# Kernel tuning notes

Hardware: AMD Instinct MI355X
Metric: run time of the kernel (lower is better)

Reference implementation:

```python
import jax, jax.numpy as jnp
import numpy as np

N, T, D, H = 100000, 16, 8, 40
HP1 = H + 1
ALPHA_DP = 1.0
KAPPA0 = 1000.0   # priorGaussianVarKappa
NU0 = 100.0       # priorWishartNu
PSI0_SCALE = 500.0  # priorWishartPsi = 500*I


def setup_inputs() -> dict:
    key = jax.random.key(0)
    ks = jax.random.split(key, 6)
    return {
        "BetaGamma1": jnp.ones((1, T), jnp.float32),
        "Phi": jax.random.uniform(ks[0], (N, T), jnp.float32),
        "inputData": jax.random.normal(ks[1], (N, D), jnp.float32),
        "outputData": jax.random.normal(ks[2], (N, 1), jnp.float32),
        "weightELM": jax.random.uniform(ks[3], (D, H), jnp.float32) * 2.0 - 1.0,
        "biasELM": jax.random.normal(ks[4], (H, 1), jnp.float32),
        "epsilonA": jnp.ones((1, T), jnp.float32),
        "epsilonB": jnp.ones((1, T), jnp.float32),
        "zetaA": 1e-4 * jnp.ones((1, T), jnp.float32),
        "zetaB": jnp.ones((1, T), jnp.float32),
    }


def reference(BetaGamma1, Phi, inputData, outputData, weightELM, biasELM,
              epsilonA, epsilonB, zetaA, zetaB):
    f32 = jnp.float32
    mu0 = jnp.zeros((D, 1), f32)                      # priorGaussianMeanMu
    Psi0 = PSI0_SCALE * jnp.eye(D, dtype=f32)         # priorWishartPsi

    sumPhi = jnp.sum(Phi, axis=0, keepdims=True)      # [1,T]

    # stick-breaking Beta params. Torch builds a flipped [T,N,T] tril mask;
    # mathematically BetaGamma2[t] = alpha + sum_{j>t} sum_n Phi[n,j]
    BetaGamma1_new = jnp.ones_like(BetaGamma1) + sumPhi
    col = sumPhi[0]                                   # [T]
    rev_incl = jnp.cumsum(col[::-1])[::-1]            # sum_{j>=t}
    BetaGamma2 = (ALPHA_DP + (rev_incl - col))[None, :]

    # Gaussian-Wishart natural-parameter updates.
    # Torch loops over clusters doing [N,D,D] bmm outer products; this is
    # S[:,:,t] = sum_n Phi[n,t] x_n x_n^T
    S = jnp.einsum('nt,ni,nj->ijt', Phi, inputData, inputData)  # [D,D,T]
    t11 = -0.5 * (Psi0 + KAPPA0 * mu0 @ mu0.T)[:, :, None] - 0.5 * S
    t12 = KAPPA0 * mu0 + inputData.T @ Phi            # [D,T]
    t21 = -0.5 * sumPhi - 0.5 * (NU0 + D + 2)         # [1,T]
    kappa = KAPPA0 + sumPhi                           # [1,T]
    mu = t12 / kappa                                  # [D,T]
    nu = -2.0 * t21 - 2.0 - float(D)                  # [1,T]
    psi = -2.0 * t11 - kappa[0][None, None, :] * jnp.einsum('it,jt->ijt', mu, mu)

    # ELM feature map + augmented design matrix X = [sigmoid(x W + b), 1]
    hmap = jax.nn.sigmoid(inputData @ weightELM + biasELM.T)   # [N,H]
    X = jnp.concatenate([hmap, jnp.ones((inputData.shape[0], 1), f32)], axis=1)  # [N,HP1]

    epsExp = (epsilonA / epsilonB)[0]                 # [T]
    zetaExp = (zetaA / zetaB)[0]                      # [T]

    # A[t] = X^T diag(Phi[:,t]) X   (torch: per-cluster bmm with diag_embed)
    A = jnp.einsum('nt,ni,nj->tij', Phi, X, X)        # [T,HP1,HP1]
    WS = jnp.linalg.inv(epsExp[:, None, None] * A
                        + zetaExp[:, None, None] * jnp.eye(HP1, dtype=f32))
    # b[t] = X^T diag(Phi[:,t]) y
    b = jnp.einsum('ni,nt->ti', X * outputData, Phi)  # [T,HP1]
    WMv = zetaExp[:, None] * jnp.einsum('tij,tj->ti', WS, b)   # [T,HP1]
    WM = WMv[:, :, None]                              # [T,HP1,1]

    # prior Zeta/Epsilon alias the variational initial values in __init__
    zetaA_new = zetaA + (H + 1) * 0.5
    zetaB_new = zetaB + 0.5 * (jnp.sum(WMv * WMv, axis=1)
                               + jnp.trace(WS, axis1=-2, axis2=-1))[None, :]
    epsA_new = epsilonA + 0.5 * sumPhi

    pred = jnp.einsum('ni,ti->tn', X, WMv)            # [T,N]
    err = outputData.T - pred                          # [T,N]
    t1 = jnp.einsum('tn,nt->t', err * err, Phi)[None, :]
    t2 = jnp.einsum('tij,tji->t', A, WS)[None, :]
    epsB_new = epsilonB + 0.5 * (t1 + t2)

    return (BetaGamma1_new, BetaGamma2, mu, kappa, nu, psi,
            WM, WS, zetaA_new, zetaB_new, epsA_new, epsB_new)
```

## Files before the change

kernel.cpp:

```cpp
#include <hip/hip_runtime.h>

#define Nn 100000
#define Tt 16
#define Dd 8
#define Hh 40
#define HP1 41

#define CSZ 53248
#define XET_OFF  0
#define XET_SZ   (64 * Nn)
#define PHIT_OFF (XET_OFF + XET_SZ)
#define PHIT_SZ  (16 * Nn)
#define ACC_OFF  (PHIT_OFF + PHIT_SZ)
#define PART_OFF (ACC_OFF + CSZ)
#define P_OFF    (PART_OFF + 8 * CSZ)

#define OFF_BG1   0
#define OFF_BG2   16
#define OFF_MU    32
#define OFF_KAPPA 160
#define OFF_NU    176
#define OFF_PSI   192
#define OFF_WM    1216
#define OFF_WS    1872
#define OFF_ZA    28768
#define OFF_ZB    28784
#define OFF_EA    28800
#define OFF_EB    28816

typedef _Float16 f16x8 __attribute__((ext_vector_type(8)));
typedef float f32x4 __attribute__((ext_vector_type(4)));
typedef unsigned short u16x8 __attribute__((ext_vector_type(8)));
typedef unsigned int u32x4 __attribute__((ext_vector_type(4)));

#define AIDX(i, t, j) ((((i) * 16 + (t)) * 64) + (j))

__global__ __launch_bounds__(256)
void elm_expand(const float* __restrict__ Phi, const float* __restrict__ Xd,
                const float* __restrict__ Yd, const float* __restrict__ W,
                const float* __restrict__ bb, unsigned int* __restrict__ XeT,
                float* __restrict__ PhiT)
{
  __shared__ float sW[Dd * Hh];
  __shared__ float sb[Hh];
  __shared__ float xs[64][9];
  __shared__ float ys[64];
  __shared__ float hrow[64][41];
  __shared__ float pt[16][68];
  int tid = threadIdx.x;
  int n0 = blockIdx.x * 64;

  for (int i = tid; i < Dd * Hh; i += 256) sW[i] = W[i];
  if (tid < Hh) sb[tid] = bb[tid];
  if (tid < 128) {
    int nl = tid >> 1, h4 = (tid & 1) * 4;
    int gn = n0 + nl;
    float4 v = (gn < Nn) ? *(const float4*)(Xd + (size_t)gn * 8 + h4)
                         : make_float4(0.f, 0.f, 0.f, 0.f);
    xs[nl][h4 + 0] = v.x; xs[nl][h4 + 1] = v.y;
    xs[nl][h4 + 2] = v.z; xs[nl][h4 + 3] = v.w;
  }
  if (tid < 64) { int gn = n0 + tid; ys[tid] = (gn < Nn) ? Yd[gn] : 0.f; }
  {
    int nl = tid >> 2, q = tid & 3;
    int gn = n0 + nl;
    float4 v = (gn < Nn) ? *(const float4*)(Phi + (size_t)gn * 16 + q * 4)
                         : make_float4(0.f, 0.f, 0.f, 0.f);
    pt[q * 4 + 0][nl] = v.x; pt[q * 4 + 1][nl] = v.y;
    pt[q * 4 + 2][nl] = v.z; pt[q * 4 + 3][nl] = v.w;
  }
  __syncthreads();
  {
    int nl = tid >> 2, hq = (tid & 3) * 10;
    for (int hh = 0; hh < 10; ++hh) {
      int h = hq + hh;
      float z = sb[h];
#pragma unroll
      for (int d = 0; d < 8; ++d) z = fmaf(xs[nl][d], sW[d * Hh + h], z);
      hrow[nl][h] = 1.f / (1.f + __expf(-z));
    }
  }
  __syncthreads();
  {
    int t = tid & 15, nq = tid >> 4;
    int gn = n0 + nq * 4;
    if (gn < Nn) {
      float4 v = make_float4(pt[t][nq * 4 + 0], pt[t][nq * 4 + 1],
                             pt[t][nq * 4 + 2], pt[t][nq * 4 + 3]);
      *(float4*)(PhiT + (size_t)t * Nn + gn) = v;
    }
  }
  {
    int c = tid >> 2, nb = (tid & 3) * 16;
    for (int q = 0; q < 4; ++q) {
      int nl = nb + q * 4;
      int gn = n0 + nl;
      if (gn >= Nn) break;
      unsigned int pu[4];
#pragma unroll
      for (int j = 0; j < 4; ++j) {
        int n = nl + j;
        float v;
        if (c < Hh) v = hrow[n][c];
        else if (c == 40) v = 1.f;
        else if (c < 49) v = xs[n][c - 41];
        else if (c == 49) v = ys[n];
        else v = 0.f;
        _Float16 hi = (_Float16)v;
        _Float16 lo = (_Float16)(v - (float)hi);
        pu[j] = ((unsigned int)__builtin_bit_cast(unsigned short, lo) << 16)
              |  (unsigned int)__builtin_bit_cast(unsigned short, hi);
      }
      *(uint4*)(XeT + (size_t)c * Nn + gn) =
          make_uint4(pu[0], pu[1], pu[2], pu[3]);
    }
  }
}

__device__ __forceinline__ void gload16(const void* g, void* l) {
  __builtin_amdgcn_global_load_lds(
      (const __attribute__((address_space(1))) unsigned int*)g,
      (__attribute__((address_space(3))) unsigned int*)l, 16, 0, 0);
}

__device__ __forceinline__ void unpack8(u32x4 a, u32x4 b, f16x8& hi, f16x8& lo) {
  u16x8 vh, vl;
#pragma unroll
  for (int e = 0; e < 4; ++e) {
    vh[e] = (unsigned short)(a[e] & 0xffffu);
    vl[e] = (unsigned short)(a[e] >> 16);
    vh[4 + e] = (unsigned short)(b[e] & 0xffffu);
    vl[4 + e] = (unsigned short)(b[e] >> 16);
  }
  hi = __builtin_bit_cast(f16x8, vh);
  lo = __builtin_bit_cast(f16x8, vl);
}

__device__ __forceinline__ void buildA(u32x4 a, u32x4 b, const float* ph,
                                       f16x8& ah, f16x8& al) {
  unsigned int u8[8];
#pragma unroll
  for (int e = 0; e < 4; ++e) { u8[e] = a[e]; u8[4 + e] = b[e]; }
#pragma unroll
  for (int e = 0; e < 8; ++e) {
    unsigned int u = u8[e];
    float hi = (float)__builtin_bit_cast(_Float16, (unsigned short)(u & 0xffffu));
    float lo = (float)__builtin_bit_cast(_Float16, (unsigned short)(u >> 16));
    float v = ph[e] * (hi + lo);
    _Float16 h = (_Float16)v;
    ah[e] = h;
    al[e] = (_Float16)(v - (float)h);
  }
}

__global__ __launch_bounds__(256, 2)
void gram_mfma(const float* __restrict__ PhiT, const unsigned int* __restrict__ XeT,
               float* __restrict__ P, int CH)
{
  __shared__ __align__(16) unsigned int xe_lds[2][2048];
  __shared__ __align__(16) float phi_lds[2][512];

  int tid = threadIdx.x;
  int l = tid & 63, w = tid >> 6;
  int lr = l >> 3, lp = l & 7;
  int gsw = lp ^ lr;
  int l15 = l & 15, lg = l >> 4;
  int bM = blockIdx.x, c = blockIdx.y;
  int n0 = c * CH;
  int rem = Nn - n0; if (rem > CH) rem = CH;
  int nsteps = rem >> 5;
  int i0 = bM * 13;

  const unsigned int* gx0 = XeT + (size_t)(16 * w + lr) * Nn + n0 + 4 * gsw;
  const unsigned int* gx1 = XeT + (size_t)(16 * w + 8 + lr) * Nn + n0 + 4 * gsw;
  const float* gp = PhiT + (size_t)(8 * w + lr) * Nn + n0 + 4 * gsw;

#define STAGE(nxt) do {                                   \
    gload16(gx0, &xe_lds[nxt][(2 * w) * 256]);            \
    gload16(gx1, &xe_lds[nxt][(2 * w + 1) * 256]);        \
    if (w < 2) gload16(gp, &phi_lds[nxt][w * 256]);       \
    gx0 += 32; gx1 += 32; gp += 32;                       \
  } while (0)

  int s1 = (2 * lg) ^ (l15 & 7), s2 = (2 * lg + 1) ^ (l15 & 7);
  int off_p0 = (l15 * 32 + 4 * s1) * 4, off_p1 = (l15 * 32 + 4 * s2) * 4;
  int off_b0[4], off_b1[4];
#pragma unroll
  for (int nt = 0; nt < 4; ++nt) {
    off_b0[nt] = ((l15 + 16 * nt) * 32 + 4 * s1) * 4;
    off_b1[nt] = ((l15 + 16 * nt) * 32 + 4 * s2) * 4;
  }
  int off_a0[4], off_a1[4];
#pragma unroll
  for (int mi = 0; mi < 4; ++mi) {
    int i = i0 + 4 * w + mi;
    int a1 = (2 * lg) ^ (i & 7), a2 = (2 * lg + 1) ^ (i & 7);
    off_a0[mi] = (i * 32 + 4 * a1) * 4;
    off_a1[mi] = (i * 32 + 4 * a2) * 4;
  }

  f32x4 acc[4][4];
#pragma unroll
  for (int mi = 0; mi < 4; ++mi)
#pragma unroll
    for (int nt = 0; nt < 4; ++nt) acc[mi][nt] = (f32x4){0.f, 0.f, 0.f, 0.f};

  STAGE(0);
  __syncthreads();

  for (int s = 0; s < nsteps; ++s) {
    int cur = s & 1;
    if (s + 1 < nsteps) STAGE(cur ^ 1);

    const char* xb = (const char*)&xe_lds[cur][0];
    const char* pb = (const char*)&phi_lds[cur][0];
    f32x4 p0 = *(const f32x4*)(pb + off_p0);
    f32x4 p1 = *(const f32x4*)(pb + off_p1);
    float ph[8] = {p0[0], p0[1], p0[2], p0[3], p1[0], p1[1], p1[2], p1[3]};

    f16x8 bh[4], bl[4];
#pragma unroll
    for (int nt = 0; nt < 4; ++nt) {
      u32x4 lo4 = *(const u32x4*)(xb + off_b0[nt]);
      u32x4 hi4 = *(const u32x4*)(xb + off_b1[nt]);
      unpack8(lo4, hi4, bh[nt], bl[nt]);
    }
#pragma unroll
    for (int mi = 0; mi < 4; ++mi) {
      u32x4 a0 = *(const u32x4*)(xb + off_a0[mi]);
      u32x4 a1 = *(const u32x4*)(xb + off_a1[mi]);
      f16x8 ah, al;
      buildA(a0, a1, ph, ah, al);
#pragma unroll
      for (int nt = 0; nt < 4; ++nt) {
        acc[mi][nt] = __builtin_amdgcn_mfma_f32_16x16x32_f16(ah, bh[nt], acc[mi][nt], 0, 0, 0);
        acc[mi][nt] = __builtin_amdgcn_mfma_f32_16x16x32_f16(ah, bl[nt], acc[mi][nt], 0, 0, 0);
        acc[mi][nt] = __builtin_amdgcn_mfma_f32_16x16x32_f16(al, bh[nt], acc[mi][nt], 0, 0, 0);
      }
    }
    __syncthreads();
  }
#undef STAGE

  float* Pc = P + (size_t)c * CSZ;
#pragma unroll
  for (int mi = 0; mi < 4; ++mi) {
    int mloc = 4 * w + mi;
    if (mloc < 13) {
      int i = i0 + mloc;
#pragma unroll
      for (int nt = 0; nt < 4; ++nt) {
        int j = nt * 16 + l15;
#pragma unroll
        for (int r = 0; r < 4; ++r)
          Pc[(i * 16 + lg * 4 + r) * 64 + j] = acc[mi][nt][r];
      }
    }
  }
}

__global__ __launch_bounds__(256)
void reduce_a(const float4* __restrict__ P4, int nchunks, float4* __restrict__ part4)
{
  int g = blockIdx.y;
  int idx = blockIdx.x * 256 + threadIdx.x;
  int per = (nchunks + 7) / 8;
  int c0 = g * per, c1 = c0 + per; if (c1 > nchunks) c1 = nchunks;
  float4 s = make_float4(0.f, 0.f, 0.f, 0.f);
  for (int cc = c0; cc < c1; ++cc) {
    float4 v = P4[(size_t)cc * (CSZ / 4) + idx];
    s.x += v.x; s.y += v.y; s.z += v.z; s.w += v.w;
  }
  part4[(size_t)g * (CSZ / 4) + idx] = s;
}

__global__ __launch_bounds__(256)
void reduce_b(const float4* __restrict__ part4, float4* __restrict__ acc4)
{
  int idx = blockIdx.x * 256 + threadIdx.x;
  float4 s = make_float4(0.f, 0.f, 0.f, 0.f);
#pragma unroll
  for (int g = 0; g < 8; ++g) {
    float4 v = part4[(size_t)g * (CSZ / 4) + idx];
    s.x += v.x; s.y += v.y; s.z += v.z; s.w += v.w;
  }
  acc4[idx] = s;
}

__global__ __launch_bounds__(256)
void finalize_kernel(const float* __restrict__ acc, const float* __restrict__ epsA,
                     const float* __restrict__ epsB, const float* __restrict__ zetA,
                     const float* __restrict__ zetB, float* __restrict__ out)
{
  int t = blockIdx.x;
  int tid = threadIdx.x;
  __shared__ float G[HP1][84];
  __shared__ float As[HP1][HP1 + 1];
  __shared__ float bs[HP1];
  __shared__ float colk[HP1];
  __shared__ float red[256];
  __shared__ float wmv[HP1];
  __shared__ float rowv[4][HP1 + 1];
  __shared__ float mus[Dd];

  float epsExp = epsA[t] / epsB[t];
  float zetaExp = zetA[t] / zetB[t];

  for (int idx = tid; idx < HP1 * HP1; idx += 256) {
    int i = idx / HP1, j = idx % HP1;
    float a = acc[AIDX(i, t, j)];
    As[i][j] = a;
    G[i][j] = epsExp * a + (i == j ? zetaExp : 0.f);
    G[i][41 + j] = (i == j) ? 1.f : 0.f;
  }
  for (int idx = tid; idx < HP1; idx += 256) {
    G[idx][82] = 0.f; G[idx][83] = 0.f;
    bs[idx] = acc[AIDX(idx, t, 49)];
  }
  __syncthreads();

  int c = tid % HP1;
  int ig = tid / HP1;
  int irow0 = ig * 7;

  for (int k = 0; k < HP1; ++k) {
    float pivinv = 1.f / G[k][k];
    if (tid >= 1 && tid <= HP1) G[k][k + tid] *= pivinv;
    if (tid < HP1) colk[tid] = (tid == k) ? 0.f : G[tid][k];
    __syncthreads();
    if (ig < 6) {
      int j = k + 1 + c;
      float pk = G[k][j];
#pragma unroll
      for (int r = 0; r < 7; ++r) {
        int i = irow0 + r;
        if (i < HP1 && i != k) G[i][j] = fmaf(-colk[i], pk, G[i][j]);
      }
    }
    __syncthreads();
  }

  for (int idx = tid; idx < HP1 * HP1; idx += 256) {
    int i = idx / HP1, j = idx % HP1;
    out[OFF_WS + (t * HP1 + i) * HP1 + j] = G[i][41 + j];
  }
  if (tid < HP1) {
    float s = 0.f;
    for (int j = 0; j < HP1; ++j) s += G[tid][41 + j] * bs[j];
    float w = zetaExp * s;
    wmv[tid] = w;
    out[OFF_WM + t * HP1 + tid] = w;
  }
  __syncthreads();
  float lt2 = 0.f;
  for (int idx = tid; idx < HP1 * HP1; idx += 256) {
    int i = idx / HP1, j = idx % HP1;
    lt2 += As[i][j] * G[i][41 + j];
  }
  red[tid] = lt2; __syncthreads();
  for (int s = 128; s > 0; s >>= 1) {
    if (tid < s) red[tid] += red[tid + s];
    __syncthreads();
  }
  float t2v = red[0];
  if (tid < HP1) {
    float w = wmv[tid];
    float aw = 0.f;
    for (int j = 0; j < HP1; ++j) aw += As[tid][j] * wmv[j];
    rowv[0][tid] = w * bs[tid];
    rowv[1][tid] = w * w;
    rowv[2][tid] = G[tid][41 + tid];
    rowv[3][tid] = w * aw;
  }
  __syncthreads();

  float sp = acc[AIDX(40, t, 40)];
  float kap = 1000.f + sp;
  float syy = acc[AIDX(49, t, 49)];

  if (tid == 0) {
    float wb = 0.f, wn = 0.f, trc = 0.f, quad = 0.f;
    for (int i = 0; i < HP1; ++i) {
      wb += rowv[0][i]; wn += rowv[1][i]; trc += rowv[2][i]; quad += rowv[3][i];
    }
    float t1 = syy - 2.f * wb + quad;
    out[OFF_BG1 + t] = 1.f + sp;
    float rest = 0.f;
    for (int u = t + 1; u < Tt; ++u) rest += acc[AIDX(40, u, 40)];
    out[OFF_BG2 + t] = 1.f + rest;
    out[OFF_KAPPA + t] = kap;
    out[OFF_NU + t] = sp + 100.f;
    out[OFF_ZA + t] = zetA[t] + 0.5f * (float)HP1;
    out[OFF_ZB + t] = zetB[t] + 0.5f * (wn + trc);
    out[OFF_EA + t] = epsA[t] + 0.5f * sp;
    out[OFF_EB + t] = epsB[t] + 0.5f * (t1 + t2v);
  }
  if (tid < Dd) {
    float m = acc[AIDX(40, t, 41 + tid)] / kap;
    mus[tid] = m;
    out[OFF_MU + tid * Tt + t] = m;
  }
  __syncthreads();
  if (tid < Dd * Dd) {
    int i = tid / Dd, j = tid % Dd;
    float S = acc[AIDX(41 + i, t, 41 + j)];
    float v = (i == j ? 500.f : 0.f) + S - kap * mus[i] * mus[j];
    out[OFF_PSI + (i * Dd + j) * Tt + t] = v;
  }
}

extern "C" void kernel_launch(void* const* d_in, const int* in_sizes, int n_in,
                              void* d_out, int out_size, void* d_ws, size_t ws_size,
                              hipStream_t stream) {
  const float* Phi = (const float*)d_in[1];
  const float* Xd  = (const float*)d_in[2];
  const float* Yd  = (const float*)d_in[3];
  const float* W   = (const float*)d_in[4];
  const float* bb  = (const float*)d_in[5];
  const float* eA  = (const float*)d_in[6];
  const float* eB  = (const float*)d_in[7];
  const float* zA  = (const float*)d_in[8];
  const float* zB  = (const float*)d_in[9];
  float* out = (float*)d_out;
  float* ws  = (float*)d_ws;

  unsigned int* XeT = (unsigned int*)(ws + XET_OFF);
  float* PhiT    = ws + PHIT_OFF;
  float* acc_red = ws + ACC_OFF;
  float* part    = ws + PART_OFF;
  float* P       = ws + P_OFF;

  long maxChunks = ((long)(ws_size / 4) - (long)P_OFF) / CSZ;
  if (maxChunks < 1) maxChunks = 1;
  long sp = (3125 + maxChunks - 1) / maxChunks;
  if (sp < 13) sp = 13;
  int CH = (int)(32 * sp);
  int KCe = (Nn + CH - 1) / CH;

  hipLaunchKernelGGL(elm_expand, dim3((Nn + 63) / 64), dim3(256), 0, stream,
                     Phi, Xd, Yd, W, bb, XeT, PhiT);
  hipLaunchKernelGGL(gram_mfma, dim3(4, KCe), dim3(256), 0, stream,
                     PhiT, XeT, P, CH);
  hipLaunchKernelGGL(reduce_a, dim3(52, 8), dim3(256), 0, stream,
                     (const float4*)P, KCe, (float4*)part);
  hipLaunchKernelGGL(reduce_b, dim3(52), dim3(256), 0, stream,
                     (const float4*)part, (float4*)acc_red);
  hipLaunchKernelGGL(finalize_kernel, dim3(Tt), dim3(256), 0, stream,
                     acc_red, eA, eB, zA, zB, out);
}
```

Before: 186.0 us.

## Split expanded features into fp32, hi and lo planes; fuse final reduction into finalize

The expand kernel now writes separate fp32, fp16-hi and fp16-lo planes, so the Gram kernel loads B fragments directly instead of unpacking them. The A side is built from fp32 times Phi using packed conversions, and only the 13 rows each block needs are staged. The grid is remapped to 1D so that chunks sharing a row block are interleaved. The reduce_b launch is removed and finalize sums the 8 partials itself. This trades extra workspace and expand-kernel write traffic for less ALU work in the inner loop and one fewer launch.

```diff
diff --git a/kernel.cpp b/kernel.cpp
--- a/kernel.cpp
+++ b/kernel.cpp
@@ -7,12 +7,11 @@
 #define HP1 41
 
 #define CSZ 53248
-#define XET_OFF  0
-#define XET_SZ   (64 * Nn)
-#define PHIT_OFF (XET_OFF + XET_SZ)
-#define PHIT_SZ  (16 * Nn)
-#define ACC_OFF  (PHIT_OFF + PHIT_SZ)
-#define PART_OFF (ACC_OFF + CSZ)
+#define XEF_OFF  0
+#define XEH_OFF  (XEF_OFF + 64 * Nn)
+#define XEL_OFF  (XEH_OFF + 32 * Nn)
+#define PHIT_OFF (XEL_OFF + 32 * Nn)
+#define PART_OFF (PHIT_OFF + 16 * Nn)
 #define P_OFF    (PART_OFF + 8 * CSZ)
 
 #define OFF_BG1   0
@@ -30,7 +29,6 @@
 
 typedef _Float16 f16x8 __attribute__((ext_vector_type(8)));
 typedef float f32x4 __attribute__((ext_vector_type(4)));
-typedef unsigned short u16x8 __attribute__((ext_vector_type(8)));
 typedef unsigned int u32x4 __attribute__((ext_vector_type(4)));
 
 #define AIDX(i, t, j) ((((i) * 16 + (t)) * 64) + (j))
@@ -38,7 +36,8 @@
 __global__ __launch_bounds__(256)
 void elm_expand(const float* __restrict__ Phi, const float* __restrict__ Xd,
                 const float* __restrict__ Yd, const float* __restrict__ W,
-                const float* __restrict__ bb, unsigned int* __restrict__ XeT,
+                const float* __restrict__ bb, float* __restrict__ XeF32,
+                unsigned short* __restrict__ XeHi, unsigned short* __restrict__ XeLo,
                 float* __restrict__ PhiT)
 {
   __shared__ float sW[Dd * Hh];
@@ -91,28 +90,52 @@
     }
   }
   {
-    int c = tid >> 2, nb = (tid & 3) * 16;
-    for (int q = 0; q < 4; ++q) {
-      int nl = nb + q * 4;
-      int gn = n0 + nl;
-      if (gn >= Nn) break;
-      unsigned int pu[4];
-#pragma unroll
-      for (int j = 0; j < 4; ++j) {
-        int n = nl + j;
-        float v;
-        if (c < Hh) v = hrow[n][c];
-        else if (c == 40) v = 1.f;
-        else if (c < 49) v = xs[n][c - 41];
-        else if (c == 49) v = ys[n];
-        else v = 0.f;
-        _Float16 hi = (_Float16)v;
-        _Float16 lo = (_Float16)(v - (float)hi);
-        pu[j] = ((unsigned int)__builtin_bit_cast(unsigned short, lo) << 16)
-              |  (unsigned int)__builtin_bit_cast(unsigned short, hi);
+    int cidx = tid >> 2, seg = tid & 3;
+    int nl0 = seg * 16;
+    float vv[16];
+#pragma unroll
+    for (int j = 0; j < 16; ++j) {
+      int n = nl0 + j;
+      float v;
+      if (cidx < Hh) v = hrow[n][cidx];
+      else if (cidx == 40) v = 1.f;
+      else if (cidx < 49) v = xs[n][cidx - 41];
+      else if (cidx == 49) v = ys[n];
+      else v = 0.f;
+      vv[j] = v;
+    }
+#pragma unroll
+    for (int q2 = 0; q2 < 4; ++q2) {
+      int gn = n0 + nl0 + q2 * 4;
+      if (gn < Nn)
+        *(float4*)(XeF32 + (size_t)cidx * Nn + gn) =
+            make_float4(vv[q2 * 4], vv[q2 * 4 + 1], vv[q2 * 4 + 2], vv[q2 * 4 + 3]);
+    }
+    unsigned short hs[16], ls[16];
+#pragma unroll
+    for (int j = 0; j < 16; ++j) {
+      _Float16 h = (_Float16)vv[j];
+      float r = vv[j] - (float)h;
+      _Float16 lo = (_Float16)r;
+      hs[j] = __builtin_bit_cast(unsigned short, h);
+      ls[j] = __builtin_bit_cast(unsigned short, lo);
+    }
+#pragma unroll
+    for (int q2 = 0; q2 < 2; ++q2) {
+      int gn = n0 + nl0 + q2 * 8;
+      if (gn < Nn) {
+        uint4 uh, ul;
+        uh.x = hs[q2*8+0] | ((unsigned)hs[q2*8+1] << 16);
+        uh.y = hs[q2*8+2] | ((unsigned)hs[q2*8+3] << 16);
+        uh.z = hs[q2*8+4] | ((unsigned)hs[q2*8+5] << 16);
+        uh.w = hs[q2*8+6] | ((unsigned)hs[q2*8+7] << 16);
+        ul.x = ls[q2*8+0] | ((unsigned)ls[q2*8+1] << 16);
+        ul.y = ls[q2*8+2] | ((unsigned)ls[q2*8+3] << 16);
+        ul.z = ls[q2*8+4] | ((unsigned)ls[q2*8+5] << 16);
+        ul.w = ls[q2*8+6] | ((unsigned)ls[q2*8+7] << 16);
+        *(uint4*)(XeHi + (size_t)cidx * Nn + gn) = uh;
+        *(uint4*)(XeLo + (size_t)cidx * Nn + gn) = ul;
       }
-      *(uint4*)(XeT + (size_t)c * Nn + gn) =
-          make_uint4(pu[0], pu[1], pu[2], pu[3]);
     }
   }
 }
@@ -123,81 +146,77 @@
       (__attribute__((address_space(3))) unsigned int*)l, 16, 0, 0);
 }
 
-__device__ __forceinline__ void unpack8(u32x4 a, u32x4 b, f16x8& hi, f16x8& lo) {
-  u16x8 vh, vl;
-#pragma unroll
-  for (int e = 0; e < 4; ++e) {
-    vh[e] = (unsigned short)(a[e] & 0xffffu);
-    vl[e] = (unsigned short)(a[e] >> 16);
-    vh[4 + e] = (unsigned short)(b[e] & 0xffffu);
-    vl[4 + e] = (unsigned short)(b[e] >> 16);
-  }
-  hi = __builtin_bit_cast(f16x8, vh);
-  lo = __builtin_bit_cast(f16x8, vl);
-}
-
-__device__ __forceinline__ void buildA(u32x4 a, u32x4 b, const float* ph,
-                                       f16x8& ah, f16x8& al) {
-  unsigned int u8[8];
-#pragma unroll
-  for (int e = 0; e < 4; ++e) { u8[e] = a[e]; u8[4 + e] = b[e]; }
-#pragma unroll
-  for (int e = 0; e < 8; ++e) {
-    unsigned int u = u8[e];
-    float hi = (float)__builtin_bit_cast(_Float16, (unsigned short)(u & 0xffffu));
-    float lo = (float)__builtin_bit_cast(_Float16, (unsigned short)(u >> 16));
-    float v = ph[e] * (hi + lo);
-    _Float16 h = (_Float16)v;
-    ah[e] = h;
-    al[e] = (_Float16)(v - (float)h);
-  }
-}
-
 __global__ __launch_bounds__(256, 2)
-void gram_mfma(const float* __restrict__ PhiT, const unsigned int* __restrict__ XeT,
-               float* __restrict__ P, int CH)
+void gram_mfma(const float* __restrict__ PhiT, const float* __restrict__ XeF32,
+               const unsigned short* __restrict__ XeHi,
+               const unsigned short* __restrict__ XeLo,
+               float* __restrict__ P, int CH, int KCe)
 {
-  __shared__ __align__(16) unsigned int xe_lds[2][2048];
-  __shared__ __align__(16) float phi_lds[2][512];
+  __shared__ __align__(16) char smem[2][12288];
+
+  int id = blockIdx.x;
+  int low3 = id & 7, rest = id >> 3;
+  int bM = rest & 3, chigh = rest >> 2;
+  int c = chigh * 8 + low3;
+  if (c >= KCe) return;
 
   int tid = threadIdx.x;
   int l = tid & 63, w = tid >> 6;
-  int lr = l >> 3, lp = l & 7;
-  int gsw = lp ^ lr;
   int l15 = l & 15, lg = l >> 4;
-  int bM = blockIdx.x, c = blockIdx.y;
   int n0 = c * CH;
   int rem = Nn - n0; if (rem > CH) rem = CH;
   int nsteps = rem >> 5;
   int i0 = bM * 13;
 
-  const unsigned int* gx0 = XeT + (size_t)(16 * w + lr) * Nn + n0 + 4 * gsw;
-  const unsigned int* gx1 = XeT + (size_t)(16 * w + 8 + lr) * Nn + n0 + 4 * gsw;
-  const float* gp = PhiT + (size_t)(8 * w + lr) * Nn + n0 + 4 * gsw;
-
-#define STAGE(nxt) do {                                   \
-    gload16(gx0, &xe_lds[nxt][(2 * w) * 256]);            \
-    gload16(gx1, &xe_lds[nxt][(2 * w + 1) * 256]);        \
-    if (w < 2) gload16(gp, &phi_lds[nxt][w * 256]);       \
-    gx0 += 32; gx1 += 32; gp += 32;                       \
+  const char* gp[3];
+  int gstep[3];
+  int ldoff[3];
+  {
+    int idq = w * 3;
+#pragma unroll
+    for (int q = 0; q < 3; ++q) {
+      int sid = idq + q;
+      ldoff[q] = sid * 1024;
+      if (sid < 8) {
+        int qq = sid & 3;
+        int row = 16 * qq + (l >> 2);
+        int g = (l & 3) ^ ((l >> 3) & 3);
+        const unsigned short* basep = (sid < 4) ? XeHi : XeLo;
+        gp[q] = (const char*)(basep + (size_t)row * Nn + n0 + 8 * g);
+        gstep[q] = 64;
+      } else if (sid < 10) {
+        int qq = sid - 8;
+        int row = 8 * qq + (l >> 3);
+        gp[q] = (const char*)(XeF32 + (size_t)(i0 + row) * Nn + n0 + 4 * (l & 7));
+        gstep[q] = 128;
+      } else {
+        int qq = sid - 10;
+        int row = 8 * qq + (l >> 3);
+        int g = (l & 7) ^ (l >> 3);
+        gp[q] = (const char*)(PhiT + (size_t)row * Nn + n0 + 4 * g);
+        gstep[q] = 128;
+      }
+    }
+  }
+
+#define STAGE(buf) do {                          \
+    char* db = &smem[buf][0];                    \
+    gload16(gp[0], db + ldoff[0]); gp[0] += gstep[0]; \
+    gload16(gp[1], db + ldoff[1]); gp[1] += gstep[1]; \
+    gload16(gp[2], db + ldoff[2]); gp[2] += gstep[2]; \
   } while (0)
 
-  int s1 = (2 * lg) ^ (l15 & 7), s2 = (2 * lg + 1) ^ (l15 & 7);
-  int off_p0 = (l15 * 32 + 4 * s1) * 4, off_p1 = (l15 * 32 + 4 * s2) * 4;
-  int off_b0[4], off_b1[4];
-#pragma unroll
-  for (int nt = 0; nt < 4; ++nt) {
-    off_b0[nt] = ((l15 + 16 * nt) * 32 + 4 * s1) * 4;
-    off_b1[nt] = ((l15 + 16 * nt) * 32 + 4 * s2) * 4;
-  }
-  int off_a0[4], off_a1[4];
-#pragma unroll
-  for (int mi = 0; mi < 4; ++mi) {
-    int i = i0 + 4 * w + mi;
-    int a1 = (2 * lg) ^ (i & 7), a2 = (2 * lg + 1) ^ (i & 7);
-    off_a0[mi] = (i * 32 + 4 * a1) * 4;
-    off_a1[mi] = (i * 32 + 4 * a2) * 4;
-  }
+  int sB = (l15 >> 1) & 3;
+  int off_b[4];
+#pragma unroll
+  for (int nt = 0; nt < 4; ++nt)
+    off_b[nt] = (l15 + 16 * nt) * 64 + 16 * (lg ^ sB);
+  int off_a[4];
+#pragma unroll
+  for (int mi = 0; mi < 4; ++mi)
+    off_a[mi] = 8192 + (4 * w + mi) * 128 + 32 * lg;
+  int off_p0 = 10240 + l15 * 128 + 16 * ((2 * lg) ^ (l15 & 7));
+  int off_p1 = 10240 + l15 * 128 + 16 * ((2 * lg + 1) ^ (l15 & 7));
 
   f32x4 acc[4][4];
 #pragma unroll
@@ -212,25 +231,41 @@
     int cur = s & 1;
     if (s + 1 < nsteps) STAGE(cur ^ 1);
 
-    const char* xb = (const char*)&xe_lds[cur][0];
-    const char* pb = (const char*)&phi_lds[cur][0];
-    f32x4 p0 = *(const f32x4*)(pb + off_p0);
-    f32x4 p1 = *(const f32x4*)(pb + off_p1);
-    float ph[8] = {p0[0], p0[1], p0[2], p0[3], p1[0], p1[1], p1[2], p1[3]};
-
+    const char* base = &smem[cur][0];
+    f32x4 p0 = *(const f32x4*)(base + off_p0);
+    f32x4 p1 = *(const f32x4*)(base + off_p1);
     f16x8 bh[4], bl[4];
 #pragma unroll
     for (int nt = 0; nt < 4; ++nt) {
-      u32x4 lo4 = *(const u32x4*)(xb + off_b0[nt]);
-      u32x4 hi4 = *(const u32x4*)(xb + off_b1[nt]);
-      unpack8(lo4, hi4, bh[nt], bl[nt]);
+      bh[nt] = *(const f16x8*)(base + off_b[nt]);
+      bl[nt] = *(const f16x8*)(base + 4096 + off_b[nt]);
     }
 #pragma unroll
     for (int mi = 0; mi < 4; ++mi) {
-      u32x4 a0 = *(const u32x4*)(xb + off_a0[mi]);
-      u32x4 a1 = *(const u32x4*)(xb + off_a1[mi]);
-      f16x8 ah, al;
-      buildA(a0, a1, ph, ah, al);
+      f32x4 x0 = *(const f32x4*)(base + off_a[mi]);
+      f32x4 x1 = *(const f32x4*)(base + off_a[mi] + 16);
+      float v0 = p0[0] * x0[0], v1 = p0[1] * x0[1];
+      float v2 = p0[2] * x0[2], v3 = p0[3] * x0[3];
+      float v4 = p1[0] * x1[0], v5 = p1[1] * x1[1];
+      float v6 = p1[2] * x1[2], v7 = p1[3] * x1[3];
+      auto h0 = __builtin_amdgcn_cvt_pkrtz(v0, v1);
+      auto h1 = __builtin_amdgcn_cvt_pkrtz(v2, v3);
+      auto h2 = __builtin_amdgcn_cvt_pkrtz(v4, v5);
+      auto h3 = __builtin_amdgcn_cvt_pkrtz(v6, v7);
+      float r0 = v0 - (float)h0[0], r1 = v1 - (float)h0[1];
+      float r2 = v2 - (float)h1[0], r3 = v3 - (float)h1[1];
+      float r4 = v4 - (float)h2[0], r5 = v5 - (float)h2[1];
+      float r6 = v6 - (float)h3[0], r7 = v7 - (float)h3[1];
+      auto e0 = __builtin_amdgcn_cvt_pkrtz(r0, r1);
+      auto e1 = __builtin_amdgcn_cvt_pkrtz(r2, r3);
+      auto e2 = __builtin_amdgcn_cvt_pkrtz(r4, r5);
+      auto e3 = __builtin_amdgcn_cvt_pkrtz(r6, r7);
+      u32x4 uh = {__builtin_bit_cast(unsigned int, h0), __builtin_bit_cast(unsigned int, h1),
+                  __builtin_bit_cast(unsigned int, h2), __builtin_bit_cast(unsigned int, h3)};
+      u32x4 ul = {__builtin_bit_cast(unsigned int, e0), __builtin_bit_cast(unsigned int, e1),
+                  __builtin_bit_cast(unsigned int, e2), __builtin_bit_cast(unsigned int, e3)};
+      f16x8 ah = __builtin_bit_cast(f16x8, uh);
+      f16x8 al = __builtin_bit_cast(f16x8, ul);
 #pragma unroll
       for (int nt = 0; nt < 4; ++nt) {
         acc[mi][nt] = __builtin_amdgcn_mfma_f32_16x16x32_f16(ah, bh[nt], acc[mi][nt], 0, 0, 0);
@@ -274,21 +309,15 @@
   part4[(size_t)g * (CSZ / 4) + idx] = s;
 }
 
+__device__ __forceinline__ float accv(const float* __restrict__ part, int idx) {
+  float s = 0.f;
+#pragma unroll
+  for (int g = 0; g < 8; ++g) s += part[g * CSZ + idx];
+  return s;
+}
+
 __global__ __launch_bounds__(256)
-void reduce_b(const float4* __restrict__ part4, float4* __restrict__ acc4)
-{
-  int idx = blockIdx.x * 256 + threadIdx.x;
-  float4 s = make_float4(0.f, 0.f, 0.f, 0.f);
-#pragma unroll
-  for (int g = 0; g < 8; ++g) {
-    float4 v = part4[(size_t)g * (CSZ / 4) + idx];
-    s.x += v.x; s.y += v.y; s.z += v.z; s.w += v.w;
-  }
-  acc4[idx] = s;
-}
-
-__global__ __launch_bounds__(256)
-void finalize_kernel(const float* __restrict__ acc, const float* __restrict__ epsA,
+void finalize_kernel(const float* __restrict__ part, const float* __restrict__ epsA,
                      const float* __restrict__ epsB, const float* __restrict__ zetA,
                      const float* __restrict__ zetB, float* __restrict__ out)
 {
@@ -308,14 +337,14 @@
 
   for (int idx = tid; idx < HP1 * HP1; idx += 256) {
     int i = idx / HP1, j = idx % HP1;
-    float a = acc[AIDX(i, t, j)];
+    float a = accv(part, AIDX(i, t, j));
     As[i][j] = a;
     G[i][j] = epsExp * a + (i == j ? zetaExp : 0.f);
     G[i][41 + j] = (i == j) ? 1.f : 0.f;
   }
   for (int idx = tid; idx < HP1; idx += 256) {
     G[idx][82] = 0.f; G[idx][83] = 0.f;
-    bs[idx] = acc[AIDX(idx, t, 49)];
+    bs[idx] = accv(part, AIDX(idx, t, 49));
   }
   __syncthreads();
 
@@ -374,9 +403,9 @@
   }
   __syncthreads();
 
-  float sp = acc[AIDX(40, t, 40)];
+  float sp = accv(part, AIDX(40, t, 40));
   float kap = 1000.f + sp;
-  float syy = acc[AIDX(49, t, 49)];
+  float syy = accv(part, AIDX(49, t, 49));
 
   if (tid == 0) {
     float wb = 0.f, wn = 0.f, trc = 0.f, quad = 0.f;
@@ -386,7 +415,7 @@
     float t1 = syy - 2.f * wb + quad;
     out[OFF_BG1 + t] = 1.f + sp;
     float rest = 0.f;
-    for (int u = t + 1; u < Tt; ++u) rest += acc[AIDX(40, u, 40)];
+    for (int u = t + 1; u < Tt; ++u) rest += accv(part, AIDX(40, u, 40));
     out[OFF_BG2 + t] = 1.f + rest;
     out[OFF_KAPPA + t] = kap;
     out[OFF_NU + t] = sp + 100.f;
@@ -396,14 +425,14 @@
     out[OFF_EB + t] = epsB[t] + 0.5f * (t1 + t2v);
   }
   if (tid < Dd) {
-    float m = acc[AIDX(40, t, 41 + tid)] / kap;
+    float m = accv(part, AIDX(40, t, 41 + tid)) / kap;
     mus[tid] = m;
     out[OFF_MU + tid * Tt + t] = m;
   }
   __syncthreads();
   if (tid < Dd * Dd) {
     int i = tid / Dd, j = tid % Dd;
-    float S = acc[AIDX(41 + i, t, 41 + j)];
+    float S = accv(part, AIDX(41 + i, t, 41 + j));
     float v = (i == j ? 500.f : 0.f) + S - kap * mus[i] * mus[j];
     out[OFF_PSI + (i * Dd + j) * Tt + t] = v;
   }
@@ -424,11 +453,12 @@
   float* out = (float*)d_out;
   float* ws  = (float*)d_ws;
 
-  unsigned int* XeT = (unsigned int*)(ws + XET_OFF);
-  float* PhiT    = ws + PHIT_OFF;
-  float* acc_red = ws + ACC_OFF;
-  float* part    = ws + PART_OFF;
-  float* P       = ws + P_OFF;
+  float* XeF32 = ws + XEF_OFF;
+  unsigned short* XeHi = (unsigned short*)(ws + XEH_OFF);
+  unsigned short* XeLo = (unsigned short*)(ws + XEL_OFF);
+  float* PhiT = ws + PHIT_OFF;
+  float* part = ws + PART_OFF;
+  float* P    = ws + P_OFF;
 
   long maxChunks = ((long)(ws_size / 4) - (long)P_OFF) / CSZ;
   if (maxChunks < 1) maxChunks = 1;
@@ -436,15 +466,14 @@
   if (sp < 13) sp = 13;
   int CH = (int)(32 * sp);
   int KCe = (Nn + CH - 1) / CH;
+  int grid1 = 32 * ((KCe + 7) / 8);
 
   hipLaunchKernelGGL(elm_expand, dim3((Nn + 63) / 64), dim3(256), 0, stream,
-                     Phi, Xd, Yd, W, bb, XeT, PhiT);
-  hipLaunchKernelGGL(gram_mfma, dim3(4, KCe), dim3(256), 0, stream,
-                     PhiT, XeT, P, CH);
+                     Phi, Xd, Yd, W, bb, XeF32, XeHi, XeLo, PhiT);
+  hipLaunchKernelGGL(gram_mfma, dim3(grid1), dim3(256), 0, stream,
+                     PhiT, XeF32, XeHi, XeLo, P, CH, KCe);
   hipLaunchKernelGGL(reduce_a, dim3(52, 8), dim3(256), 0, stream,
                      (const float4*)P, KCe, (float4*)part);
-  hipLaunchKernelGGL(reduce_b, dim3(52), dim3(256), 0, stream,
-                     (const float4*)part, (float4*)acc_red);
   hipLaunchKernelGGL(finalize_kernel, dim3(Tt), dim3(256), 0, stream,
-                     acc_red, eA, eB, zA, zB, out);
-}
+                     part, eA, eB, zA, zB, out);
+}
```

Measured after the change: 177.6 us. -4.5%, faster.
